# Optimization experiments

Measured on AMD Instinct MI355X. Metric: run time of the kernel, lower is better.

Reference implementation:

```python
import jax, jax.numpy as jnp
import numpy as np
import math

NUM_HEADS = 12


def setup_inputs() -> dict:
    key = jax.random.key(0)
    ks = jax.random.split(key, 9)
    R, L, B, E = 128, 512, 1, 768
    s = 1.0 / math.sqrt(E)
    return {
        "x": jax.random.normal(ks[0], (R, L, B, E), dtype=jnp.float32),
        "wq": jax.random.normal(ks[1], (E, E), dtype=jnp.float32) * s,
        "bq": jax.random.normal(ks[2], (E,), dtype=jnp.float32) * 0.02,
        "wk": jax.random.normal(ks[3], (E, E), dtype=jnp.float32) * s,
        "bk": jax.random.normal(ks[4], (E,), dtype=jnp.float32) * 0.02,
        "wv": jax.random.normal(ks[5], (E, E), dtype=jnp.float32) * s,
        "bv": jax.random.normal(ks[6], (E,), dtype=jnp.float32) * 0.02,
        "wo": jax.random.normal(ks[7], (E, E), dtype=jnp.float32) * s,
        "bo": jax.random.normal(ks[8], (E,), dtype=jnp.float32) * 0.02,
    }


def reference(x, wq, bq, wk, bk, wv, bv, wo, bo):
    # x: [num_rows, num_cols, batch, embed_dim]
    R, L, B, E = x.shape
    H = NUM_HEADS
    D = E // H
    # scaling = head_dim**-0.5 / sqrt(num_rows)  (align_scaling)
    scaling = (D ** -0.5) / math.sqrt(R)

    q = (x @ wq.T + bq).reshape(R, L, B, H, D) * scaling
    k = (x @ wk.T + bk).reshape(R, L, B, H, D)
    v = (x @ wv.T + bv).reshape(R, L, B, H, D)

    # row attention: contract over rows r and head_dim d -> logits [h, n, i, j]
    attn_weights = jnp.einsum("rinhd,rjnhd->hnij", q, k)
    attn_probs = jax.nn.softmax(attn_weights, axis=-1)

    context = jnp.einsum("hnij,rjnhd->rinhd", attn_probs, v)
    context = context.reshape(R, L, B, E)
    output = context @ wo.T + bo
    return (output, attn_probs)
```

## Files before the change

kernel.cpp:

```cpp
#include <hip/hip_runtime.h>
#include <hip/hip_bf16.h>

typedef unsigned short u16;
typedef u16   u16x4 __attribute__((ext_vector_type(4)));
typedef u16   u16x8 __attribute__((ext_vector_type(8)));
typedef short bf16x8 __attribute__((ext_vector_type(8)));
typedef float f32x4 __attribute__((ext_vector_type(4)));

#define R_    128
#define L_    512
#define E_    768
#define H_    12
#define RD_   8192
#define M_    65536
#define OUT0_N 50331648
#define PART_ 3145728

__device__ __forceinline__ u16 rne_bf16(float f) {
  unsigned u = __builtin_bit_cast(unsigned, f);
  u += 0x7FFFu + ((u >> 16) & 1u);
  return (u16)(u >> 16);
}

__device__ __forceinline__ void gload_lds16(const u16* g, u16* l) {
  __builtin_amdgcn_global_load_lds(
      (const __attribute__((address_space(1))) void*)g,
      (__attribute__((address_space(3))) void*)l, 16, 0, 0);
}

__device__ __forceinline__ int xcd_remap(int d, int nwg) {
  return (d & 7) * (nwg >> 3) + (d >> 3);
}

__device__ __forceinline__ void gemm_core256(
    const u16* __restrict__ Ab, const u16* __restrict__ Bb,
    const int lda, const int ldb, const int K,
    u16* sm, f32x4 acc[8][4])
{
  const int t    = threadIdx.x;
  const int lane = t & 63;
  const int w    = t >> 6;
  const int wm   = (w >> 2) << 7;
  const int wn   = (w & 3) << 6;
  const int frow = lane & 15;

  const int crow  = t >> 3;
  const int gslot = (t & 7) ^ (crow & 7);
  const u16* gA = Ab + (size_t)crow * lda + (gslot << 3);
  const u16* gB = Bb + (size_t)crow * ldb + (gslot << 3);
  const int stg = t << 3;

  const int rd0 = (((lane >> 4)    ) ^ (lane & 7)) << 3;
  const int rd1 = (((lane >> 4) | 4) ^ (lane & 7)) << 3;

#define STG_A(c_, buf_, ko_) \
  gload_lds16(gA + (ko_) + (size_t)((c_) << 6) * lda, (buf_) + ((c_) << 12) + stg)
#define STG_B(c_, buf_, ko_) \
  gload_lds16(gB + (ko_) + (size_t)((c_) << 6) * ldb, (buf_) + 16384 + ((c_) << 12) + stg)

  const int nt = K >> 6;
  STG_B(0, sm, 0); STG_B(1, sm, 0); STG_B(2, sm, 0); STG_B(3, sm, 0);
  STG_A(0, sm, 0); STG_A(2, sm, 0); STG_A(1, sm, 0); STG_A(3, sm, 0);
  asm volatile("s_waitcnt vmcnt(2)" ::: "memory");
  __builtin_amdgcn_s_barrier();

  for (int tt = 0; tt < nt; ++tt) {
    u16* bufc = sm + ((tt & 1) << 15);
    u16* bufn = sm + (((tt + 1) & 1) << 15);
    const bool st = (tt + 1 < nt);
    const int ko = (tt + 1) << 6;

    bf16x8 af[4], bff[4];
#pragma unroll
    for (int b = 0; b < 4; ++b)
      bff[b] = *(const bf16x8*)(bufc + 16384 + ((wn + b * 16 + frow) << 6) + rd0);
#pragma unroll
    for (int a = 0; a < 4; ++a)
      af[a] = *(const bf16x8*)(bufc + ((wm + a * 16 + frow) << 6) + rd0);
    if (st) { STG_B(0, bufn, ko); STG_B(1, bufn, ko); }
    __builtin_amdgcn_s_barrier();
    __builtin_amdgcn_s_setprio(1);
#pragma unroll
    for (int a = 0; a < 4; ++a)
#pragma unroll
      for (int b = 0; b < 4; ++b)
        acc[a][b] = __builtin_amdgcn_mfma_f32_16x16x32_bf16(af[a], bff[b], acc[a][b], 0, 0, 0);
    __builtin_amdgcn_s_setprio(0);
    if (st) asm volatile("s_waitcnt vmcnt(2)" ::: "memory");
    else    asm volatile("s_waitcnt vmcnt(0)" ::: "memory");
    __builtin_amdgcn_s_barrier();

#pragma unroll
    for (int a = 0; a < 4; ++a)
      af[a] = *(const bf16x8*)(bufc + ((wm + (a + 4) * 16 + frow) << 6) + rd0);
    if (st) { STG_B(2, bufn, ko); STG_B(3, bufn, ko); }
    __builtin_amdgcn_s_barrier();
    __builtin_amdgcn_s_setprio(1);
#pragma unroll
    for (int a = 0; a < 4; ++a)
#pragma unroll
      for (int b = 0; b < 4; ++b)
        acc[a + 4][b] = __builtin_amdgcn_mfma_f32_16x16x32_bf16(af[a], bff[b], acc[a + 4][b], 0, 0, 0);
    __builtin_amdgcn_s_setprio(0);
    __builtin_amdgcn_s_barrier();

#pragma unroll
    for (int b = 0; b < 4; ++b)
      bff[b] = *(const bf16x8*)(bufc + 16384 + ((wn + b * 16 + frow) << 6) + rd1);
#pragma unroll
    for (int a = 0; a < 4; ++a)
      af[a] = *(const bf16x8*)(bufc + ((wm + a * 16 + frow) << 6) + rd1);
    if (st) { STG_A(0, bufn, ko); STG_A(2, bufn, ko); }
    __builtin_amdgcn_s_barrier();
    __builtin_amdgcn_s_setprio(1);
#pragma unroll
    for (int a = 0; a < 4; ++a)
#pragma unroll
      for (int b = 0; b < 4; ++b)
        acc[a][b] = __builtin_amdgcn_mfma_f32_16x16x32_bf16(af[a], bff[b], acc[a][b], 0, 0, 0);
    __builtin_amdgcn_s_setprio(0);
    __builtin_amdgcn_s_barrier();

#pragma unroll
    for (int a = 0; a < 4; ++a)
      af[a] = *(const bf16x8*)(bufc + ((wm + (a + 4) * 16 + frow) << 6) + rd1);
    if (st) { STG_A(1, bufn, ko); STG_A(3, bufn, ko); }
    __builtin_amdgcn_s_barrier();
    __builtin_amdgcn_s_setprio(1);
#pragma unroll
    for (int a = 0; a < 4; ++a)
#pragma unroll
      for (int b = 0; b < 4; ++b)
        acc[a + 4][b] = __builtin_amdgcn_mfma_f32_16x16x32_bf16(af[a], bff[b], acc[a + 4][b], 0, 0, 0);
    __builtin_amdgcn_s_setprio(0);
    if (st) asm volatile("s_waitcnt vmcnt(2)" ::: "memory");
    __builtin_amdgcn_s_barrier();
  }
#undef STG_A
#undef STG_B
}

#define EPILOGUE_IDX256                           \
  const int lane = threadIdx.x & 63;              \
  const int w    = threadIdx.x >> 6;              \
  const int wm   = (w >> 2) << 7;                 \
  const int wn   = (w & 3) << 6;                  \
  const int row4 = (lane >> 4) << 2;              \
  const int coll = lane & 15;

#define ACC_INIT256                               \
  f32x4 acc[8][4];                                \
  {                                               \
    f32x4 zz = {0.0f, 0.0f, 0.0f, 0.0f};          \
    _Pragma("unroll")                             \
    for (int a = 0; a < 8; ++a)                   \
      _Pragma("unroll")                           \
      for (int b = 0; b < 4; ++b) acc[a][b] = zz; \
  }

__device__ __forceinline__ void gemm_core(
    const u16* __restrict__ Ab, const u16* __restrict__ Bb,
    const int lda, const int ldb, const int K,
    u16* sm, f32x4 acc[4][4])
{
  const int t    = threadIdx.x;
  const int lane = t & 63;
  const int w    = t >> 6;
  const int wm   = (w >> 1) << 6;
  const int wn   = (w & 1) << 6;
  const int frow = lane & 15;

  const int srow = (w << 3) + (lane >> 3);
  const int scol = ((lane & 7) ^ (lane >> 3)) << 3;
  const u16* gA = Ab + (size_t)srow * lda + scol;
  const u16* gB = Bb + (size_t)srow * ldb + scol;
  const int stg_l = (w << 9) + (lane << 3);

#pragma unroll
  for (int j = 0; j < 4; ++j) {
    gload_lds16(gA + (size_t)(j << 5) * lda, sm + (j << 11) + stg_l);
    gload_lds16(gB + (size_t)(j << 5) * ldb, sm + 8192 + (j << 11) + stg_l);
  }

  const int nt = K >> 6;
  for (int tt = 0; tt < nt; ++tt) {
    const int cur = tt & 1;
    u16* bufc = sm + (cur << 14);
    u16* bufn = sm + ((cur ^ 1) << 14);
    __builtin_amdgcn_s_barrier();
    if (tt + 1 < nt) {
      const u16* gA1 = gA + ((size_t)(tt + 1) << 6);
      const u16* gB1 = gB + ((size_t)(tt + 1) << 6);
#pragma unroll
      for (int j = 0; j < 4; ++j) {
        gload_lds16(gA1 + (size_t)(j << 5) * lda, bufn + (j << 11) + stg_l);
        gload_lds16(gB1 + (size_t)(j << 5) * ldb, bufn + 8192 + (j << 11) + stg_l);
      }
      asm volatile("s_waitcnt vmcnt(8)" ::: "memory");
    } else {
      asm volatile("s_waitcnt vmcnt(0)" ::: "memory");
    }
    __builtin_amdgcn_s_barrier();
    const u16* sA = bufc;
    const u16* sB = bufc + 8192;
#pragma unroll
    for (int kk = 0; kk < 2; ++kk) {
      const int rdcol = (((kk << 2) + (lane >> 4)) ^ (lane & 7)) << 3;
      bf16x8 af[4], bff[4];
#pragma unroll
      for (int a = 0; a < 4; ++a)
        af[a] = *(const bf16x8*)(sA + ((wm + a * 16 + frow) << 6) + rdcol);
#pragma unroll
      for (int b = 0; b < 4; ++b)
        bff[b] = *(const bf16x8*)(sB + ((wn + b * 16 + frow) << 6) + rdcol);
#pragma unroll
      for (int a = 0; a < 4; ++a)
#pragma unroll
        for (int b = 0; b < 4; ++b)
          acc[a][b] = __builtin_amdgcn_mfma_f32_16x16x32_bf16(af[a], bff[b], acc[a][b], 0, 0, 0);
    }
  }
}

#define EPILOGUE_IDX                              \
  const int lane = threadIdx.x & 63;              \
  const int w    = threadIdx.x >> 6;              \
  const int wm   = (w >> 1) << 6;                 \
  const int wn   = (w & 1) << 6;                  \
  const int row4 = (lane >> 4) << 2;              \
  const int coll = lane & 15;

#define ACC_INIT                                  \
  f32x4 acc[4][4];                                \
  {                                               \
    f32x4 zz = {0.0f, 0.0f, 0.0f, 0.0f};          \
    _Pragma("unroll")                             \
    for (int a = 0; a < 4; ++a)                   \
      _Pragma("unroll")                           \
      for (int b = 0; b < 4; ++b) acc[a][b] = zz; \
  }

__global__ __launch_bounds__(512) void k_gemm_qkv(
    const u16* __restrict__ xbf, const u16* __restrict__ wqkv,
    const float* __restrict__ bq, const float* __restrict__ bk,
    const float* __restrict__ bv,
    u16* __restrict__ qt, u16* __restrict__ kt, u16* __restrict__ vt2,
    const float scaling)
{
  __shared__ __align__(16) u16 smem[65536];
  const int d0 = blockIdx.x + 9 * blockIdx.y;
  const int l  = xcd_remap(d0, 2304);
  const int bn = l % 9;
  const int bm = l / 9;
  ACC_INIT256;
  gemm_core256(xbf + (size_t)bm * 256 * E_, wqkv + (size_t)bn * 256 * E_,
               E_, E_, E_, smem, acc);
  EPILOGUE_IDX256;
  const int which = bn / 3;
  const int c0 = (bn % 3) << 8;
  const float* bias = (which == 0) ? bq : (which == 1) ? bk : bv;

  if (which < 2) {
    u16* dst = (which == 0) ? qt : kt;
    const float mult = (which == 0) ? scaling : 1.0f;
#pragma unroll
    for (int a = 0; a < 8; ++a) {
#pragma unroll
      for (int b = 0; b < 4; ++b) {
        const int c = c0 + wn + b * 16 + coll;
        const int h = c >> 6, d = c & 63;
        const float bias_v = bias[c];
#pragma unroll
        for (int r = 0; r < 4; ++r) {
          const int m = (bm << 8) + wm + a * 16 + row4 + r;
          const int rr = m >> 9, i = m & 511;
          const float v = (acc[a][b][r] + bias_v) * mult;
          dst[((size_t)(h * 512 + i) << 13) + (rr << 6) + d] = rne_bf16(v);
        }
      }
    }
  } else {
    const int rr = bm >> 1;
    const int j0 = (bm & 1) << 8;
    const int wq4 = w & 3;
    for (int p = 0; p < 4; ++p) {
      __syncthreads();
      if (wq4 == p) {
#pragma unroll
        for (int a = 0; a < 8; ++a) {
          const int ml = wm + a * 16 + row4;
#pragma unroll
          for (int b = 0; b < 4; ++b) {
            const int c = c0 + wn + b * 16 + coll;
            const int nl = b * 16 + coll;
            const float bias_v = bias[c];
            u16x4 pk;
#pragma unroll
            for (int r = 0; r < 4; ++r) pk[r] = rne_bf16(acc[a][b][r] + bias_v);
            *(u16x4*)(smem + nl * 264 + ml) = pk;
          }
        }
      }
      __syncthreads();
      for (int idx = threadIdx.x; idx < 2048; idx += 512) {
        const int nl = idx >> 5, seg = idx & 31;
        const int c = c0 + (p << 6) + nl;
        const int h = c >> 6, d = c & 63;
        u16x8 vdat = *(const u16x8*)(smem + nl * 264 + (seg << 3));
        *(u16x8*)(vt2 + ((size_t)((h << 13) + (rr << 6) + d) << 9) + j0 + (seg << 3)) = vdat;
      }
    }
  }
}

__global__ __launch_bounds__(256) void k_gemm_logits(
    const u16* __restrict__ qt, const u16* __restrict__ kt,
    float* __restrict__ lgp)
{
  __shared__ __align__(16) u16 smem[32768];
  const int d0 = blockIdx.x + 4 * blockIdx.y + 16 * blockIdx.z;
  const int l  = xcd_remap(d0, 768);
  const int bm = l & 3, bn = (l >> 2) & 3;
  const int hk = l >> 4;
  const int h  = hk >> 2, ks = hk & 3;
  ACC_INIT;
  const u16* A = qt + ((size_t)h << 22) + ((size_t)bm << 20) + (ks << 11);
  const u16* B = kt + ((size_t)h << 22) + ((size_t)bn << 20) + (ks << 11);
  gemm_core(A, B, RD_, RD_, 2048, smem, acc);
  EPILOGUE_IDX;
  float* dst = lgp + ((size_t)(ks * 12 + h) << 18);
#pragma unroll
  for (int a = 0; a < 4; ++a)
#pragma unroll
    for (int b = 0; b < 4; ++b) {
      const int j = bn * 128 + wn + b * 16 + coll;
#pragma unroll
      for (int r = 0; r < 4; ++r) {
        const int i = bm * 128 + wm + a * 16 + row4 + r;
        dst[((size_t)i << 9) + j] = acc[a][b][r];
      }
    }
}

__global__ __launch_bounds__(256) void k_softmax(
    const float* __restrict__ lgp, float* __restrict__ probs,
    u16* __restrict__ pbf)
{
  const int row = blockIdx.x;
  const size_t base = (size_t)row << 9;
  const int t = threadIdx.x;
  const int lane = t & 63, w = t >> 6;
  float x0 = (lgp[base + t]       + lgp[PART_ + base + t])
           + (lgp[2 * (size_t)PART_ + base + t]       + lgp[3 * (size_t)PART_ + base + t]);
  float x1 = (lgp[base + t + 256] + lgp[PART_ + base + t + 256])
           + (lgp[2 * (size_t)PART_ + base + t + 256] + lgp[3 * (size_t)PART_ + base + t + 256]);
  float m = fmaxf(x0, x1);
#pragma unroll
  for (int off = 32; off > 0; off >>= 1) m = fmaxf(m, __shfl_xor(m, off, 64));
  __shared__ float red[8];
  if (lane == 0) red[w] = m;
  __syncthreads();
  m = fmaxf(fmaxf(red[0], red[1]), fmaxf(red[2], red[3]));
  float e0 = __expf(x0 - m), e1 = __expf(x1 - m);
  float s = e0 + e1;
#pragma unroll
  for (int off = 32; off > 0; off >>= 1) s += __shfl_xor(s, off, 64);
  if (lane == 0) red[4 + w] = s;
  __syncthreads();
  s = (red[4] + red[5]) + (red[6] + red[7]);
  const float inv = 1.0f / s;
  const float p0 = e0 * inv, p1 = e1 * inv;
  probs[base + t] = p0;
  probs[base + t + 256] = p1;
  pbf[base + t]       = rne_bf16(p0);
  pbf[base + t + 256] = rne_bf16(p1);
}

__global__ __launch_bounds__(512) void k_gemm_ctx(
    const u16* __restrict__ pbf, const u16* __restrict__ vt2,
    u16* __restrict__ ctx)
{
  __shared__ __align__(16) u16 smem[65536];
  const int d0 = blockIdx.x + (blockIdx.y << 6);
  const int l  = xcd_remap(d0, 768);
  const int bm = l & 1, bn = (l >> 1) & 31, h = l >> 6;
  ACC_INIT256;
  const u16* A = pbf + ((size_t)h << 18) + ((size_t)bm << 17);
  const u16* B = vt2 + ((size_t)h << 22) + ((size_t)bn << 17);
  gemm_core256(A, B, 512, 512, 512, smem, acc);
  EPILOGUE_IDX256;
#pragma unroll
  for (int a = 0; a < 8; ++a)
#pragma unroll
    for (int b = 0; b < 4; ++b) {
      const int n = (bn << 8) + wn + b * 16 + coll;
      const int rr = n >> 6, d = n & 63;
#pragma unroll
      for (int r = 0; r < 4; ++r) {
        const int i = (bm << 8) + wm + a * 16 + row4 + r;
        ctx[(size_t)((rr << 9) + i) * E_ + (h << 6) + d] = rne_bf16(acc[a][b][r]);
      }
    }
}

__global__ __launch_bounds__(512) void k_gemm_out(
    const u16* __restrict__ ctx, const u16* __restrict__ wob,
    const float* __restrict__ bo, float* __restrict__ out0)
{
  __shared__ __align__(16) u16 smem[65536];
  const int d0 = blockIdx.x + 3 * blockIdx.y;
  const int l  = xcd_remap(d0, 768);
  const int bn = l % 3;
  const int bm = l / 3;
  ACC_INIT256;
  gemm_core256(ctx + (size_t)bm * 256 * E_, wob + (size_t)bn * 256 * E_,
               E_, E_, E_, smem, acc);
  EPILOGUE_IDX256;
#pragma unroll
  for (int a = 0; a < 8; ++a)
#pragma unroll
    for (int b = 0; b < 4; ++b) {
      const int n = (bn << 8) + wn + b * 16 + coll;
      const float bias_v = bo[n];
#pragma unroll
      for (int r = 0; r < 4; ++r) {
        const int m = (bm << 8) + wm + a * 16 + row4 + r;
        out0[(size_t)m * E_ + n] = acc[a][b][r] + bias_v;
      }
    }
}

__device__ __forceinline__ u16x4 cvt4(float4 v) {
  u16x4 o;
  o.x = rne_bf16(v.x); o.y = rne_bf16(v.y);
  o.z = rne_bf16(v.z); o.w = rne_bf16(v.w);
  return o;
}

__global__ __launch_bounds__(256) void k_cvt_x(
    const float4* __restrict__ src, u16x4* __restrict__ dst, const int n4)
{
  const int stride = gridDim.x * blockDim.x;
  for (int i = blockIdx.x * blockDim.x + threadIdx.x; i < n4; i += stride)
    dst[i] = cvt4(src[i]);
}

__global__ __launch_bounds__(256) void k_cvt_w(
    const float4* __restrict__ wq, const float4* __restrict__ wk,
    const float4* __restrict__ wv, const float4* __restrict__ wo,
    u16x4* __restrict__ wqkv, u16x4* __restrict__ wob)
{
  const int n4 = (E_ * E_) / 4;
  const int stride = gridDim.x * blockDim.x;
  for (int i = blockIdx.x * blockDim.x + threadIdx.x; i < n4; i += stride) {
    wqkv[i]            = cvt4(wq[i]);
    wqkv[n4 + i]       = cvt4(wk[i]);
    wqkv[2 * n4 + i]   = cvt4(wv[i]);
    wob[i]             = cvt4(wo[i]);
  }
}

__global__ void k_ws_too_small(float* out0) {
  if (threadIdx.x == 0 && blockIdx.x == 0) out0[0] = 1.0e9f;
}

extern "C" void kernel_launch(void* const* d_in, const int* in_sizes, int n_in,
                              void* d_out, int out_size, void* d_ws, size_t ws_size,
                              hipStream_t stream)
{
  const float* x  = (const float*)d_in[0];
  const float* wq = (const float*)d_in[1];
  const float* bq = (const float*)d_in[2];
  const float* wk = (const float*)d_in[3];
  const float* bk = (const float*)d_in[4];
  const float* wv = (const float*)d_in[5];
  const float* bv = (const float*)d_in[6];
  const float* wo = (const float*)d_in[7];
  const float* bo = (const float*)d_in[8];

  float* out0 = (float*)d_out;
  float* outp = out0 + (size_t)OUT0_N;

  const size_t off_xbf   = 0;
  const size_t off_qt    = 100663296;
  const size_t off_kt    = 201326592;
  const size_t off_vt    = 301989888;
  const size_t off_pbf   = 402653184;
  const size_t off_wqkv  = 408944640;
  const size_t off_wob   = 412483584;
  const size_t need      = 413663232;

  if (ws_size < need) {
    k_ws_too_small<<<1, 64, 0, stream>>>(out0);
    return;
  }

  char* ws = (char*)d_ws;
  u16* xbf  = (u16*)(ws + off_xbf);
  float* lgp = (float*)(ws + off_xbf);
  u16* qt   = (u16*)(ws + off_qt);
  u16* kt   = (u16*)(ws + off_kt);
  u16* vt2  = (u16*)(ws + off_vt);
  u16* pbf  = (u16*)(ws + off_pbf);
  u16* wqkv = (u16*)(ws + off_wqkv);
  u16* wob  = (u16*)(ws + off_wob);

  const float scaling = 0.011048543456039806f;

  k_cvt_x<<<2048, 256, 0, stream>>>((const float4*)x, (u16x4*)xbf, OUT0_N / 4);
  k_cvt_w<<<192, 256, 0, stream>>>((const float4*)wq, (const float4*)wk,
                                   (const float4*)wv, (const float4*)wo,
                                   (u16x4*)wqkv, (u16x4*)wob);
  k_gemm_qkv<<<dim3(9, 256), 512, 0, stream>>>(xbf, wqkv, bq, bk, bv,
                                               qt, kt, vt2, scaling);
  k_gemm_logits<<<dim3(4, 4, 48), 256, 0, stream>>>(qt, kt, lgp);
  k_softmax<<<6144, 256, 0, stream>>>(lgp, outp, pbf);
  k_gemm_ctx<<<dim3(64, 12), 512, 0, stream>>>(pbf, vt2, xbf );
  k_gemm_out<<<dim3(3, 256), 512, 0, stream>>>(xbf, wob, bo, out0);
}
```

Measured before the change: 601.3 us.

## Fuse fp32-to-bf16 conversion of x into QKV GEMM and use nontemporal stores

Removes the separate k_cvt_x pass and adds a GEMM core that loads fp32 x tiles directly, converts them to bf16 in registers and writes them into swizzled LDS, while B tiles still stream through global_load_lds. This drops a full read and write of the 200MB fp32 activation tensor. Large output writes (logits, probs, V transpose, final output) become nontemporal stores to reduce cache pollution, and the QKV kernel gets a launch-bounds occupancy hint. In exchange, A loads go through registers, which adds VGPR pressure and conversion ALU work inside the GEMM loop.

```diff
diff --git a/kernel.cpp b/kernel.cpp
--- a/kernel.cpp
+++ b/kernel.cpp
@@ -22,6 +22,15 @@
   return (u16)(u >> 16);
 }
 
+__device__ __forceinline__ unsigned pack2(float a, float b) {
+  return (unsigned)rne_bf16(a) | ((unsigned)rne_bf16(b) << 16);
+}
+
+template <typename T>
+__device__ __forceinline__ void nt_store(T* p, T v) {
+  __builtin_nontemporal_store(v, p);
+}
+
 __device__ __forceinline__ void gload_lds16(const u16* g, u16* l) {
   __builtin_amdgcn_global_load_lds(
       (const __attribute__((address_space(1))) void*)g,
@@ -30,6 +39,135 @@
 
 __device__ __forceinline__ int xcd_remap(int d, int nwg) {
   return (d & 7) * (nwg >> 3) + (d >> 3);
+}
+
+__device__ __forceinline__ void gemm_core256_f32a(
+    const float* __restrict__ Af, const u16* __restrict__ Bb,
+    const int lda_f, const int ldb, const int K,
+    u16* sm, f32x4 acc[8][4])
+{
+  const int t    = threadIdx.x;
+  const int lane = t & 63;
+  const int w    = t >> 6;
+  const int wm   = (w >> 2) << 7;
+  const int wn   = (w & 3) << 6;
+  const int frow = lane & 15;
+
+  const int crow  = t >> 3;
+  const int gslot = (t & 7) ^ (crow & 7);
+  const u16* gB = Bb + (size_t)crow * ldb + (gslot << 3);
+  const int stg = t << 3;
+
+  const int arow = t >> 4;
+  const float* gA = Af + (size_t)arow * lda_f + ((t & 15) << 2);
+  const int s_log = (t & 15) >> 1;
+  const int aswz  = ((s_log ^ (arow & 7)) << 3) + ((t & 1) << 2);
+
+  const int rd0 = (((lane >> 4)    ) ^ (lane & 7)) << 3;
+  const int rd1 = (((lane >> 4) | 4) ^ (lane & 7)) << 3;
+
+#define LD_A(q_, ko_) (*(const float4*)(gA + (size_t)((q_) << 5) * lda_f + (ko_)))
+#define WR_A(q_, f_, buf_)                                               \
+  {                                                                      \
+    uint2 pk_;                                                           \
+    pk_.x = pack2((f_).x, (f_).y);                                       \
+    pk_.y = pack2((f_).z, (f_).w);                                       \
+    *(uint2*)((buf_) + ((((q_) << 5) + arow) << 6) + aswz) = pk_;        \
+  }
+#define STG_B(c_, buf_, ko_) \
+  gload_lds16(gB + (ko_) + (size_t)((c_) << 6) * ldb, (buf_) + 16384 + ((c_) << 12) + stg)
+
+  const int nt = K >> 6;
+  {
+    float4 fa0 = LD_A(0, 0), fa1 = LD_A(1, 0), fa2 = LD_A(2, 0), fa3 = LD_A(3, 0);
+    float4 fb0 = LD_A(4, 0), fb1 = LD_A(5, 0), fb2 = LD_A(6, 0), fb3 = LD_A(7, 0);
+    STG_B(0, sm, 0); STG_B(1, sm, 0); STG_B(2, sm, 0); STG_B(3, sm, 0);
+    WR_A(0, fa0, sm); WR_A(1, fa1, sm); WR_A(2, fa2, sm); WR_A(3, fa3, sm);
+    WR_A(4, fb0, sm); WR_A(5, fb1, sm); WR_A(6, fb2, sm); WR_A(7, fb3, sm);
+    asm volatile("s_waitcnt vmcnt(0) lgkmcnt(0)" ::: "memory");
+    __builtin_amdgcn_s_barrier();
+  }
+
+  for (int tt = 0; tt < nt; ++tt) {
+    u16* bufc = sm + ((tt & 1) << 15);
+    u16* bufn = sm + (((tt + 1) & 1) << 15);
+    const bool st = (tt + 1 < nt);
+    const int ko = (tt + 1) << 6;
+
+    bf16x8 af[4], bff[4];
+    float4 fa0, fa1, fa2, fa3, fb0, fb1, fb2, fb3;
+
+#pragma unroll
+    for (int b = 0; b < 4; ++b)
+      bff[b] = *(const bf16x8*)(bufc + 16384 + ((wn + b * 16 + frow) << 6) + rd0);
+#pragma unroll
+    for (int a = 0; a < 4; ++a)
+      af[a] = *(const bf16x8*)(bufc + ((wm + a * 16 + frow) << 6) + rd0);
+    if (st) { fa0 = LD_A(0, ko); fa1 = LD_A(1, ko); fa2 = LD_A(2, ko); fa3 = LD_A(3, ko); }
+    __builtin_amdgcn_s_barrier();
+    __builtin_amdgcn_s_setprio(1);
+#pragma unroll
+    for (int a = 0; a < 4; ++a)
+#pragma unroll
+      for (int b = 0; b < 4; ++b)
+        acc[a][b] = __builtin_amdgcn_mfma_f32_16x16x32_bf16(af[a], bff[b], acc[a][b], 0, 0, 0);
+    __builtin_amdgcn_s_setprio(0);
+    __builtin_amdgcn_s_barrier();
+
+#pragma unroll
+    for (int a = 0; a < 4; ++a)
+      af[a] = *(const bf16x8*)(bufc + ((wm + (a + 4) * 16 + frow) << 6) + rd0);
+    if (st) {
+      fb0 = LD_A(4, ko); fb1 = LD_A(5, ko); fb2 = LD_A(6, ko); fb3 = LD_A(7, ko);
+      WR_A(0, fa0, bufn); WR_A(1, fa1, bufn); WR_A(2, fa2, bufn); WR_A(3, fa3, bufn);
+    }
+    __builtin_amdgcn_s_barrier();
+    __builtin_amdgcn_s_setprio(1);
+#pragma unroll
+    for (int a = 0; a < 4; ++a)
+#pragma unroll
+      for (int b = 0; b < 4; ++b)
+        acc[a + 4][b] = __builtin_amdgcn_mfma_f32_16x16x32_bf16(af[a], bff[b], acc[a + 4][b], 0, 0, 0);
+    __builtin_amdgcn_s_setprio(0);
+    __builtin_amdgcn_s_barrier();
+
+#pragma unroll
+    for (int b = 0; b < 4; ++b)
+      bff[b] = *(const bf16x8*)(bufc + 16384 + ((wn + b * 16 + frow) << 6) + rd1);
+#pragma unroll
+    for (int a = 0; a < 4; ++a)
+      af[a] = *(const bf16x8*)(bufc + ((wm + a * 16 + frow) << 6) + rd1);
+    if (st) {
+      STG_B(0, bufn, ko); STG_B(1, bufn, ko); STG_B(2, bufn, ko); STG_B(3, bufn, ko);
+      WR_A(4, fb0, bufn); WR_A(5, fb1, bufn); WR_A(6, fb2, bufn); WR_A(7, fb3, bufn);
+    }
+    __builtin_amdgcn_s_barrier();
+    __builtin_amdgcn_s_setprio(1);
+#pragma unroll
+    for (int a = 0; a < 4; ++a)
+#pragma unroll
+      for (int b = 0; b < 4; ++b)
+        acc[a][b] = __builtin_amdgcn_mfma_f32_16x16x32_bf16(af[a], bff[b], acc[a][b], 0, 0, 0);
+    __builtin_amdgcn_s_setprio(0);
+    __builtin_amdgcn_s_barrier();
+
+#pragma unroll
+    for (int a = 0; a < 4; ++a)
+      af[a] = *(const bf16x8*)(bufc + ((wm + (a + 4) * 16 + frow) << 6) + rd1);
+    __builtin_amdgcn_s_barrier();
+    __builtin_amdgcn_s_setprio(1);
+#pragma unroll
+    for (int a = 0; a < 4; ++a)
+#pragma unroll
+      for (int b = 0; b < 4; ++b)
+        acc[a + 4][b] = __builtin_amdgcn_mfma_f32_16x16x32_bf16(af[a], bff[b], acc[a + 4][b], 0, 0, 0);
+    __builtin_amdgcn_s_setprio(0);
+    asm volatile("s_waitcnt vmcnt(0) lgkmcnt(0)" ::: "memory");
+    __builtin_amdgcn_s_barrier();
+  }
+#undef LD_A
+#undef WR_A
+#undef STG_B
 }
 
 __device__ __forceinline__ void gemm_core256(
@@ -240,8 +378,8 @@
       for (int b = 0; b < 4; ++b) acc[a][b] = zz; \
   }
 
-__global__ __launch_bounds__(512) void k_gemm_qkv(
-    const u16* __restrict__ xbf, const u16* __restrict__ wqkv,
+__global__ __launch_bounds__(512, 2) void k_gemm_qkv(
+    const float* __restrict__ xf, const u16* __restrict__ wqkv,
     const float* __restrict__ bq, const float* __restrict__ bk,
     const float* __restrict__ bv,
     u16* __restrict__ qt, u16* __restrict__ kt, u16* __restrict__ vt2,
@@ -253,8 +391,8 @@
   const int bn = l % 9;
   const int bm = l / 9;
   ACC_INIT256;
-  gemm_core256(xbf + (size_t)bm * 256 * E_, wqkv + (size_t)bn * 256 * E_,
-               E_, E_, E_, smem, acc);
+  gemm_core256_f32a(xf + (size_t)bm * 256 * E_, wqkv + (size_t)bn * 256 * E_,
+                    E_, E_, E_, smem, acc);
   EPILOGUE_IDX256;
   const int which = bn / 3;
   const int c0 = (bn % 3) << 8;
@@ -307,7 +445,7 @@
         const int c = c0 + (p << 6) + nl;
         const int h = c >> 6, d = c & 63;
         u16x8 vdat = *(const u16x8*)(smem + nl * 264 + (seg << 3));
-        *(u16x8*)(vt2 + ((size_t)((h << 13) + (rr << 6) + d) << 9) + j0 + (seg << 3)) = vdat;
+        nt_store((u16x8*)(vt2 + ((size_t)((h << 13) + (rr << 6) + d) << 9) + j0 + (seg << 3)), vdat);
       }
     }
   }
@@ -337,7 +475,7 @@
 #pragma unroll
       for (int r = 0; r < 4; ++r) {
         const int i = bm * 128 + wm + a * 16 + row4 + r;
-        dst[((size_t)i << 9) + j] = acc[a][b][r];
+        nt_store(&dst[((size_t)i << 9) + j], acc[a][b][r]);
       }
     }
 }
@@ -370,8 +508,8 @@
   s = (red[4] + red[5]) + (red[6] + red[7]);
   const float inv = 1.0f / s;
   const float p0 = e0 * inv, p1 = e1 * inv;
-  probs[base + t] = p0;
-  probs[base + t + 256] = p1;
+  nt_store(&probs[base + t], p0);
+  nt_store(&probs[base + t + 256], p1);
   pbf[base + t]       = rne_bf16(p0);
   pbf[base + t + 256] = rne_bf16(p1);
 }
@@ -425,7 +563,7 @@
 #pragma unroll
       for (int r = 0; r < 4; ++r) {
         const int m = (bm << 8) + wm + a * 16 + row4 + r;
-        out0[(size_t)m * E_ + n] = acc[a][b][r] + bias_v;
+        nt_store(&out0[(size_t)m * E_ + n], acc[a][b][r] + bias_v);
       }
     }
 }
@@ -435,14 +573,6 @@
   o.x = rne_bf16(v.x); o.y = rne_bf16(v.y);
   o.z = rne_bf16(v.z); o.w = rne_bf16(v.w);
   return o;
-}
-
-__global__ __launch_bounds__(256) void k_cvt_x(
-    const float4* __restrict__ src, u16x4* __restrict__ dst, const int n4)
-{
-  const int stride = gridDim.x * blockDim.x;
-  for (int i = blockIdx.x * blockDim.x + threadIdx.x; i < n4; i += stride)
-    dst[i] = cvt4(src[i]);
 }
 
 __global__ __launch_bounds__(256) void k_cvt_w(
@@ -481,7 +611,7 @@
   float* out0 = (float*)d_out;
   float* outp = out0 + (size_t)OUT0_N;
 
-  const size_t off_xbf   = 0;
+  const size_t off_lgp   = 0;
   const size_t off_qt    = 100663296;
   const size_t off_kt    = 201326592;
   const size_t off_vt    = 301989888;
@@ -496,8 +626,8 @@
   }
 
   char* ws = (char*)d_ws;
-  u16* xbf  = (u16*)(ws + off_xbf);
-  float* lgp = (float*)(ws + off_xbf);
+  float* lgp = (float*)(ws + off_lgp);
+  u16* ctxb = (u16*)(ws + off_lgp);
   u16* qt   = (u16*)(ws + off_qt);
   u16* kt   = (u16*)(ws + off_kt);
   u16* vt2  = (u16*)(ws + off_vt);
@@ -507,14 +637,13 @@
 
   const float scaling = 0.011048543456039806f;
 
-  k_cvt_x<<<2048, 256, 0, stream>>>((const float4*)x, (u16x4*)xbf, OUT0_N / 4);
   k_cvt_w<<<192, 256, 0, stream>>>((const float4*)wq, (const float4*)wk,
                                    (const float4*)wv, (const float4*)wo,
                                    (u16x4*)wqkv, (u16x4*)wob);
-  k_gemm_qkv<<<dim3(9, 256), 512, 0, stream>>>(xbf, wqkv, bq, bk, bv,
+  k_gemm_qkv<<<dim3(9, 256), 512, 0, stream>>>(x, wqkv, bq, bk, bv,
                                                qt, kt, vt2, scaling);
   k_gemm_logits<<<dim3(4, 4, 48), 256, 0, stream>>>(qt, kt, lgp);
   k_softmax<<<6144, 256, 0, stream>>>(lgp, outp, pbf);
-  k_gemm_ctx<<<dim3(64, 12), 512, 0, stream>>>(pbf, vt2, xbf );
-  k_gemm_out<<<dim3(3, 256), 512, 0, stream>>>(xbf, wob, bo, out0);
-}
+  k_gemm_ctx<<<dim3(64, 12), 512, 0, stream>>>(pbf, vt2, ctxb);
+  k_gemm_out<<<dim3(3, 256), 512, 0, stream>>>(ctxb, wob, bo, out0);
+}
```

New measurement: 683.9 us. +13.7%, slower.
